# Optimization experiments

Measured on AMD Instinct MI355X. Metric: run time of the kernel, lower is better.

## Reference

```python
import jax, jax.numpy as jnp
import numpy as np

D = 1024
K = 256
B = 8192


def setup_inputs() -> dict:
    key = jax.random.key(0)
    kx, kw, kd, kp = jax.random.split(key, 4)
    x = jax.random.normal(kx, (B, D), dtype=jnp.float32)
    # scale weights ~1/sqrt(d) so the 11-matmul chain stays numerically sane
    Ws = jax.random.normal(kw, (10, D, D), dtype=jnp.float32) / jnp.sqrt(jnp.float32(D))
    W_dec = jax.random.normal(kd, (D, K), dtype=jnp.float32) / jnp.sqrt(jnp.float32(K))
    perm = jax.random.randint(kp, (K,), 0, D, dtype=jnp.int64)
    return {"x": x, "Ws": Ws, "W_dec": W_dec, "perm": perm}


def reference(x, Ws, W_dec, perm):
    # torch nn.Linear(d,d,bias=False): y = x @ W.T
    # source applies fc1..fc9, then fc9 AGAIN, then fc10 (11 matmuls, 10 weights)
    order = list(range(9)) + [8, 9]
    h = x
    for i in order:
        h = h @ Ws[i].T  # [B, D]
    y = h[:, perm]        # vectorized gather, replaces per-row python loop [B, K]
    out = y @ W_dec.T     # fc_decode: [B, D]
    return out
```

## Files before the change

kernel.cpp:

```cpp
#include <hip/hip_runtime.h>
#include <stdint.h>
#include <stddef.h>

typedef __bf16 bf16;
typedef __bf16 bf16x8 __attribute__((ext_vector_type(8)));
typedef float f32x4 __attribute__((ext_vector_type(4)));

__device__ __forceinline__ void global_to_lds16(const void* g, void* l) {
  const __attribute__((address_space(1))) unsigned* gp =
      reinterpret_cast<const __attribute__((address_space(1))) unsigned*>(
          reinterpret_cast<uintptr_t>(g));
  __attribute__((address_space(3))) unsigned* lp =
      reinterpret_cast<__attribute__((address_space(3))) unsigned*>(
          reinterpret_cast<uintptr_t>(l));
  __builtin_amdgcn_global_load_lds(gp, lp, 16, 0, 0);
}

struct PrepArgs {
  const float* cvt_src[5]; bf16* cvt_dst[5];
  const float* tr_src[6];  bf16* tr_dst[6];
  const float* x; bf16* xbf;
  const float* Wdec; const int* praw; bf16* Gbf;
};

__global__ __launch_bounds__(256) void prep_all(PrepArgs p) {
  __shared__ alignas(16) char smem[64 * 65 * 2];
  const int b = blockIdx.x;
  const int tid = threadIdx.x;

  if (b < 2560) {
    const int m = b >> 9, blk = b & 511;
    const float* __restrict__ src = p.cvt_src[m];
    bf16* __restrict__ dst = p.cvt_dst[m];
    const int i = (blk * 256 + tid) * 8;
    float4 a = *(const float4*)(src + i);
    float4 c = *(const float4*)(src + i + 4);
    bf16x8 o;
    o[0] = (bf16)a.x; o[1] = (bf16)a.y; o[2] = (bf16)a.z; o[3] = (bf16)a.w;
    o[4] = (bf16)c.x; o[5] = (bf16)c.y; o[6] = (bf16)c.z; o[7] = (bf16)c.w;
    *(bf16x8*)(dst + i) = o;
  } else if (b < 4096) {
    const int t = b - 2560;
    const int m = t >> 8, r = t & 255;
    const float* __restrict__ src = p.tr_src[m];
    bf16* __restrict__ dst = p.tr_dst[m];
    bf16(*tile)[65] = reinterpret_cast<bf16(*)[65]>(smem);
    const int bx = (r & 15) * 64;
    const int by = (r >> 4) * 64;
    const int tx = tid & 63;
    const int ty4 = tid >> 6;
#pragma unroll
    for (int rr = 0; rr < 16; rr++) {
      int row = ty4 * 16 + rr;
      tile[row][tx] = (bf16)src[(size_t)(by + row) * 1024 + bx + tx];
    }
    __syncthreads();
#pragma unroll
    for (int rr = 0; rr < 16; rr++) {
      int row = ty4 * 16 + rr;
      dst[(size_t)(bx + row) * 1024 + by + tx] = tile[tx][row];
    }
  } else if (b < 8192) {
    const int blk = b - 4096;
    const int i = (blk * 256 + tid) * 8;
    float4 a = *(const float4*)(p.x + i);
    float4 c = *(const float4*)(p.x + i + 4);
    bf16x8 o;
    o[0] = (bf16)a.x; o[1] = (bf16)a.y; o[2] = (bf16)a.z; o[3] = (bf16)a.w;
    o[4] = (bf16)c.x; o[5] = (bf16)c.y; o[6] = (bf16)c.z; o[7] = (bf16)c.w;
    *(bf16x8*)(p.xbf + i) = o;
  } else {
    const int j = b - 8192;
    float* row = (float*)smem;
    int* perm_l = (int*)(smem + 4096);
    int* nzp = (int*)(smem + 4096 + 1024);
#pragma unroll
    for (int c = 0; c < 4; c++) row[tid * 4 + c] = 0.f;
    if (tid == 0) *nzp = 0;
    __syncthreads();
    if (tid < 128 && p.praw[2 * tid + 1] != 0) atomicOr(nzp, 1);
    __syncthreads();
    const int is64 = (*nzp == 0);
    perm_l[tid] = is64 ? p.praw[2 * tid] : p.praw[tid];
    __syncthreads();
    atomicAdd(&row[perm_l[tid]], p.Wdec[(size_t)j * 256 + tid]);
    __syncthreads();
#pragma unroll
    for (int c = 0; c < 4; c++)
      p.Gbf[(size_t)j * 1024 + tid * 4 + c] = (bf16)row[tid * 4 + c];
  }
}

struct GemmBatch { const bf16* A[6]; const bf16* B[6]; bf16* C[6]; };

__global__ __launch_bounds__(256) void gemm64_nt(GemmBatch bt) {
  const bf16* __restrict__ A = bt.A[blockIdx.z];
  const bf16* __restrict__ B = bt.B[blockIdx.z];
  bf16* __restrict__ C = bt.C[blockIdx.z];

  __shared__ bf16 As[64 * 32];
  __shared__ bf16 Bs[64 * 32];

  const int tid = threadIdx.x;
  const int wave = tid >> 6, lane = tid & 63;
  const int quad = lane >> 4, l16 = lane & 15;
  const int rowBase = blockIdx.y * 64;
  const int colBase = blockIdx.x * 64;
  const int waveM = (wave >> 1) * 32, waveN = (wave & 1) * 32;

  const int e = tid * 8;
  const int sr = e >> 5, sc = e & 31;
  const bf16* Ag = A + (size_t)(rowBase + sr) * 1024 + sc;
  const bf16* Bg = B + (size_t)(colBase + sr) * 1024 + sc;
  char* AsB = (char*)As + wave * 1024;
  char* BsB = (char*)Bs + wave * 1024;

  f32x4 acc[2][2] = {};

  for (int k0 = 0; k0 < 1024; k0 += 32) {
    global_to_lds16(Ag + k0, AsB);
    global_to_lds16(Bg + k0, BsB);
    __syncthreads();
    bf16x8 af[2], bfr[2];
#pragma unroll
    for (int mi = 0; mi < 2; mi++)
      af[mi] = *(const bf16x8*)(As + (waveM + mi * 16 + l16) * 32 + quad * 8);
#pragma unroll
    for (int ni = 0; ni < 2; ni++)
      bfr[ni] = *(const bf16x8*)(Bs + (waveN + ni * 16 + l16) * 32 + quad * 8);
#pragma unroll
    for (int mi = 0; mi < 2; mi++)
#pragma unroll
      for (int ni = 0; ni < 2; ni++)
        acc[mi][ni] = __builtin_amdgcn_mfma_f32_16x16x32_bf16(af[mi], bfr[ni],
                                                              acc[mi][ni], 0, 0, 0);
    __syncthreads();
  }

  bf16* Cb = C + (size_t)(rowBase + waveM) * 1024 + colBase + waveN;
#pragma unroll
  for (int mi = 0; mi < 2; mi++)
#pragma unroll
    for (int ni = 0; ni < 2; ni++)
#pragma unroll
      for (int r = 0; r < 4; r++)
        Cb[(size_t)(mi * 16 + quad * 4 + r) * 1024 + ni * 16 + l16] =
            (bf16)acc[mi][ni][r];
}

__global__ __launch_bounds__(256) void gemm128_nt_f32(const bf16* __restrict__ A,
                                                      const bf16* __restrict__ B,
                                                      float* __restrict__ C) {
  __shared__ bf16 As[128 * 32];
  __shared__ bf16 Bs[128 * 32];

  const int tid = threadIdx.x;
  const int wave = tid >> 6, lane = tid & 63;
  const int quad = lane >> 4, l16 = lane & 15;
  const int rowBase = blockIdx.y * 128;
  const int colBase = blockIdx.x * 128;
  const int waveM = (wave >> 1) * 64, waveN = (wave & 1) * 64;

  const int e = tid * 8;
  const int sr = e >> 5, sc = e & 31;
  const bf16* Ag0 = A + (size_t)(rowBase + sr) * 1024 + sc;
  const bf16* Ag1 = Ag0 + (size_t)64 * 1024;
  const bf16* Bg0 = B + (size_t)(colBase + sr) * 1024 + sc;
  const bf16* Bg1 = Bg0 + (size_t)64 * 1024;
  char* AsB0 = (char*)As + wave * 1024;
  char* AsB1 = AsB0 + 4096;
  char* BsB0 = (char*)Bs + wave * 1024;
  char* BsB1 = BsB0 + 4096;

  f32x4 acc[4][4] = {};

  for (int k0 = 0; k0 < 1024; k0 += 32) {
    global_to_lds16(Ag0 + k0, AsB0);
    global_to_lds16(Ag1 + k0, AsB1);
    global_to_lds16(Bg0 + k0, BsB0);
    global_to_lds16(Bg1 + k0, BsB1);
    __syncthreads();
    bf16x8 af[4], bfr[4];
#pragma unroll
    for (int mi = 0; mi < 4; mi++)
      af[mi] = *(const bf16x8*)(As + (waveM + mi * 16 + l16) * 32 + quad * 8);
#pragma unroll
    for (int ni = 0; ni < 4; ni++)
      bfr[ni] = *(const bf16x8*)(Bs + (waveN + ni * 16 + l16) * 32 + quad * 8);
#pragma unroll
    for (int mi = 0; mi < 4; mi++)
#pragma unroll
      for (int ni = 0; ni < 4; ni++)
        acc[mi][ni] = __builtin_amdgcn_mfma_f32_16x16x32_bf16(af[mi], bfr[ni],
                                                              acc[mi][ni], 0, 0, 0);
    __syncthreads();
  }

  float* Cb = C + (size_t)(rowBase + waveM) * 1024 + colBase + waveN;
#pragma unroll
  for (int mi = 0; mi < 4; mi++)
#pragma unroll
    for (int ni = 0; ni < 4; ni++)
#pragma unroll
      for (int r = 0; r < 4; r++)
        Cb[(size_t)(mi * 16 + quad * 4 + r) * 1024 + ni * 16 + l16] =
            acc[mi][ni][r];
}

extern "C" void kernel_launch(void* const* d_in, const int* in_sizes, int n_in,
                              void* d_out, int out_size, void* d_ws, size_t ws_size,
                              hipStream_t stream) {
  const float* x    = (const float*)d_in[0];
  const float* Wsrc = (const float*)d_in[1];
  const float* Wdec = (const float*)d_in[2];
  const int*   praw = (const int*)d_in[3];
  float* out = (float*)d_out;

  constexpr size_t MAT  = 1024ull * 1024ull;
  constexpr size_t SLOT = 2ull * 1024 * 1024;

  char* ws = (char*)d_ws;
  bf16* Wrm[5];
  for (int i = 0; i < 5; i++) Wrm[i] = (bf16*)(ws + (size_t)i * SLOT);
  bf16* Wt[6];
  for (int i = 0; i < 6; i++) Wt[i] = (bf16*)(ws + (size_t)(5 + i) * SLOT);
  bf16* Gbf = (bf16*)(ws + 11 * SLOT);
  bf16* xbf = (bf16*)(ws + 12 * SLOT);
  bf16* P[6];
  for (int i = 0; i < 6; i++) P[i] = (bf16*)(ws + (size_t)(20 + i) * SLOT);
  bf16* Q[3];
  for (int i = 0; i < 3; i++) Q[i] = (bf16*)(ws + (size_t)(26 + i) * SLOT);
  bf16* Rb = (bf16*)(ws + 29 * SLOT);
  bf16* Fb = (bf16*)(ws + 30 * SLOT);

  PrepArgs pa;
  const int rmIdx[5] = {1, 3, 5, 7, 8};
  for (int i = 0; i < 5; i++) { pa.cvt_src[i] = Wsrc + (size_t)rmIdx[i] * MAT; pa.cvt_dst[i] = Wrm[i]; }
  const int trIdx[6] = {0, 2, 4, 6, 8, 9};
  for (int i = 0; i < 6; i++) { pa.tr_src[i] = Wsrc + (size_t)trIdx[i] * MAT; pa.tr_dst[i] = Wt[i]; }
  pa.x = x; pa.xbf = xbf; pa.Wdec = Wdec; pa.praw = praw; pa.Gbf = Gbf;
  prep_all<<<dim3(9216), 256, 0, stream>>>(pa);

  GemmBatch L1;
  const bf16* l1a[6] = {Gbf, Wt[4], Wrm[3], Wt[2], Wrm[1], Wt[0]};
  const bf16* l1b[6] = {Wt[5], Wrm[4], Wt[3], Wrm[2], Wt[1], Wrm[0]};
  for (int i = 0; i < 6; i++) { L1.A[i] = l1a[i]; L1.B[i] = l1b[i]; L1.C[i] = P[i]; }
  gemm64_nt<<<dim3(16, 16, 6), 256, 0, stream>>>(L1);

  GemmBatch L2;
  const bf16* l2a[3] = {P[0], P[3], P[5]};
  const bf16* l2b[3] = {P[1], P[2], P[4]};
  for (int i = 0; i < 3; i++) { L2.A[i] = l2a[i]; L2.B[i] = l2b[i]; L2.C[i] = Q[i]; }
  gemm64_nt<<<dim3(16, 16, 3), 256, 0, stream>>>(L2);

  GemmBatch L3{};
  L3.A[0] = Q[0]; L3.B[0] = Q[1]; L3.C[0] = Rb;
  gemm64_nt<<<dim3(16, 16, 1), 256, 0, stream>>>(L3);

  GemmBatch L4{};
  L4.A[0] = Rb; L4.B[0] = Q[2]; L4.C[0] = Fb;
  gemm64_nt<<<dim3(16, 16, 1), 256, 0, stream>>>(L4);

  gemm128_nt_f32<<<dim3(8, 64), 256, 0, stream>>>(xbf, Fb, out);

  (void)in_sizes; (void)n_in; (void)out_size; (void)ws_size;
}
```

Measured before the change: 222.5 us.

## Use 128x128 tiles for weight-chain GEMMs and fold x conversion into first GEMM launch

The weight-product tree GEMMs move from 64x64 tiles to the shared 128x128 MFMA body, which raises data reuse per block. The catch is far fewer blocks: 64 per 1024x1024 product, on a device with many CUs. The fp32-to-bf16 conversion of x is moved out of the prep kernel and into the first-level GEMM launch as trailing blocks. The aim is to overlap that memory-bound work with the compute-bound GEMM blocks. The risk is poor GPU occupancy in the serial L3/L4 stages, where only 64 blocks run.

```diff
diff --git a/kernel.cpp b/kernel.cpp
--- a/kernel.cpp
+++ b/kernel.cpp
@@ -16,10 +16,70 @@
   __builtin_amdgcn_global_load_lds(gp, lp, 16, 0, 0);
 }
 
+template <typename OutT>
+__device__ __forceinline__ void gemm128_body(const bf16* __restrict__ A,
+                                             const bf16* __restrict__ B,
+                                             OutT* __restrict__ C,
+                                             int bx, int by) {
+  __shared__ bf16 As[128 * 32];
+  __shared__ bf16 Bs[128 * 32];
+
+  const int tid = threadIdx.x;
+  const int wave = tid >> 6, lane = tid & 63;
+  const int quad = lane >> 4, l16 = lane & 15;
+  const int rowBase = by * 128;
+  const int colBase = bx * 128;
+  const int waveM = (wave >> 1) * 64, waveN = (wave & 1) * 64;
+
+  const int e = tid * 8;
+  const int sr = e >> 5, sc = e & 31;
+  const bf16* Ag0 = A + (size_t)(rowBase + sr) * 1024 + sc;
+  const bf16* Ag1 = Ag0 + (size_t)64 * 1024;
+  const bf16* Bg0 = B + (size_t)(colBase + sr) * 1024 + sc;
+  const bf16* Bg1 = Bg0 + (size_t)64 * 1024;
+  char* AsB0 = (char*)As + wave * 1024;
+  char* AsB1 = AsB0 + 4096;
+  char* BsB0 = (char*)Bs + wave * 1024;
+  char* BsB1 = BsB0 + 4096;
+
+  f32x4 acc[4][4] = {};
+
+  for (int k0 = 0; k0 < 1024; k0 += 32) {
+    global_to_lds16(Ag0 + k0, AsB0);
+    global_to_lds16(Ag1 + k0, AsB1);
+    global_to_lds16(Bg0 + k0, BsB0);
+    global_to_lds16(Bg1 + k0, BsB1);
+    __syncthreads();
+    bf16x8 af[4], bfr[4];
+#pragma unroll
+    for (int mi = 0; mi < 4; mi++)
+      af[mi] = *(const bf16x8*)(As + (waveM + mi * 16 + l16) * 32 + quad * 8);
+#pragma unroll
+    for (int ni = 0; ni < 4; ni++)
+      bfr[ni] = *(const bf16x8*)(Bs + (waveN + ni * 16 + l16) * 32 + quad * 8);
+#pragma unroll
+    for (int mi = 0; mi < 4; mi++)
+#pragma unroll
+      for (int ni = 0; ni < 4; ni++)
+        acc[mi][ni] = __builtin_amdgcn_mfma_f32_16x16x32_bf16(af[mi], bfr[ni],
+                                                              acc[mi][ni], 0, 0, 0);
+    __syncthreads();
+  }
+
+  OutT* Cb = C + (size_t)(rowBase + waveM) * 1024 + colBase + waveN;
+#pragma unroll
+  for (int mi = 0; mi < 4; mi++)
+#pragma unroll
+    for (int ni = 0; ni < 4; ni++)
+#pragma unroll
+      for (int r = 0; r < 4; r++)
+        Cb[(size_t)(mi * 16 + quad * 4 + r) * 1024 + ni * 16 + l16] =
+            (OutT)acc[mi][ni][r];
+}
+
 struct PrepArgs {
   const float* cvt_src[5]; bf16* cvt_dst[5];
   const float* tr_src[6];  bf16* tr_dst[6];
-  const float* x; bf16* xbf;
   const float* Wdec; const int* praw; bf16* Gbf;
 };
 
@@ -60,17 +120,8 @@
       int row = ty4 * 16 + rr;
       dst[(size_t)(bx + row) * 1024 + by + tx] = tile[tx][row];
     }
-  } else if (b < 8192) {
-    const int blk = b - 4096;
-    const int i = (blk * 256 + tid) * 8;
-    float4 a = *(const float4*)(p.x + i);
-    float4 c = *(const float4*)(p.x + i + 4);
-    bf16x8 o;
-    o[0] = (bf16)a.x; o[1] = (bf16)a.y; o[2] = (bf16)a.z; o[3] = (bf16)a.w;
-    o[4] = (bf16)c.x; o[5] = (bf16)c.y; o[6] = (bf16)c.z; o[7] = (bf16)c.w;
-    *(bf16x8*)(p.xbf + i) = o;
   } else {
-    const int j = b - 8192;
+    const int j = b - 4096;
     float* row = (float*)smem;
     int* perm_l = (int*)(smem + 4096);
     int* nzp = (int*)(smem + 4096 + 1024);
@@ -91,120 +142,39 @@
   }
 }
 
-struct GemmBatch { const bf16* A[6]; const bf16* B[6]; bf16* C[6]; };
-
-__global__ __launch_bounds__(256) void gemm64_nt(GemmBatch bt) {
-  const bf16* __restrict__ A = bt.A[blockIdx.z];
-  const bf16* __restrict__ B = bt.B[blockIdx.z];
-  bf16* __restrict__ C = bt.C[blockIdx.z];
-
-  __shared__ bf16 As[64 * 32];
-  __shared__ bf16 Bs[64 * 32];
-
-  const int tid = threadIdx.x;
-  const int wave = tid >> 6, lane = tid & 63;
-  const int quad = lane >> 4, l16 = lane & 15;
-  const int rowBase = blockIdx.y * 64;
-  const int colBase = blockIdx.x * 64;
-  const int waveM = (wave >> 1) * 32, waveN = (wave & 1) * 32;
-
-  const int e = tid * 8;
-  const int sr = e >> 5, sc = e & 31;
-  const bf16* Ag = A + (size_t)(rowBase + sr) * 1024 + sc;
-  const bf16* Bg = B + (size_t)(colBase + sr) * 1024 + sc;
-  char* AsB = (char*)As + wave * 1024;
-  char* BsB = (char*)Bs + wave * 1024;
-
-  f32x4 acc[2][2] = {};
-
-  for (int k0 = 0; k0 < 1024; k0 += 32) {
-    global_to_lds16(Ag + k0, AsB);
-    global_to_lds16(Bg + k0, BsB);
-    __syncthreads();
-    bf16x8 af[2], bfr[2];
-#pragma unroll
-    for (int mi = 0; mi < 2; mi++)
-      af[mi] = *(const bf16x8*)(As + (waveM + mi * 16 + l16) * 32 + quad * 8);
-#pragma unroll
-    for (int ni = 0; ni < 2; ni++)
-      bfr[ni] = *(const bf16x8*)(Bs + (waveN + ni * 16 + l16) * 32 + quad * 8);
-#pragma unroll
-    for (int mi = 0; mi < 2; mi++)
-#pragma unroll
-      for (int ni = 0; ni < 2; ni++)
-        acc[mi][ni] = __builtin_amdgcn_mfma_f32_16x16x32_bf16(af[mi], bfr[ni],
-                                                              acc[mi][ni], 0, 0, 0);
-    __syncthreads();
+struct L1Args {
+  const bf16* A[6]; const bf16* B[6]; bf16* C[6];
+  const float* x; bf16* xbf;
+};
+
+__global__ __launch_bounds__(256) void l1_gemm_xcvt(L1Args a) {
+  const int b = blockIdx.x;
+  if (b < 384) {
+    const int z = b >> 6, t = b & 63;
+    gemm128_body<bf16>(a.A[z], a.B[z], a.C[z], t & 7, t >> 3);
+  } else {
+    const int i = ((b - 384) * 256 + (int)threadIdx.x) * 8;
+    float4 v0 = *(const float4*)(a.x + i);
+    float4 v1 = *(const float4*)(a.x + i + 4);
+    bf16x8 o;
+    o[0] = (bf16)v0.x; o[1] = (bf16)v0.y; o[2] = (bf16)v0.z; o[3] = (bf16)v0.w;
+    o[4] = (bf16)v1.x; o[5] = (bf16)v1.y; o[6] = (bf16)v1.z; o[7] = (bf16)v1.w;
+    *(bf16x8*)(a.xbf + i) = o;
   }
-
-  bf16* Cb = C + (size_t)(rowBase + waveM) * 1024 + colBase + waveN;
-#pragma unroll
-  for (int mi = 0; mi < 2; mi++)
-#pragma unroll
-    for (int ni = 0; ni < 2; ni++)
-#pragma unroll
-      for (int r = 0; r < 4; r++)
-        Cb[(size_t)(mi * 16 + quad * 4 + r) * 1024 + ni * 16 + l16] =
-            (bf16)acc[mi][ni][r];
-}
-
-__global__ __launch_bounds__(256) void gemm128_nt_f32(const bf16* __restrict__ A,
-                                                      const bf16* __restrict__ B,
-                                                      float* __restrict__ C) {
-  __shared__ bf16 As[128 * 32];
-  __shared__ bf16 Bs[128 * 32];
-
-  const int tid = threadIdx.x;
-  const int wave = tid >> 6, lane = tid & 63;
-  const int quad = lane >> 4, l16 = lane & 15;
-  const int rowBase = blockIdx.y * 128;
-  const int colBase = blockIdx.x * 128;
-  const int waveM = (wave >> 1) * 64, waveN = (wave & 1) * 64;
-
-  const int e = tid * 8;
-  const int sr = e >> 5, sc = e & 31;
-  const bf16* Ag0 = A + (size_t)(rowBase + sr) * 1024 + sc;
-  const bf16* Ag1 = Ag0 + (size_t)64 * 1024;
-  const bf16* Bg0 = B + (size_t)(colBase + sr) * 1024 + sc;
-  const bf16* Bg1 = Bg0 + (size_t)64 * 1024;
-  char* AsB0 = (char*)As + wave * 1024;
-  char* AsB1 = AsB0 + 4096;
-  char* BsB0 = (char*)Bs + wave * 1024;
-  char* BsB1 = BsB0 + 4096;
-
-  f32x4 acc[4][4] = {};
-
-  for (int k0 = 0; k0 < 1024; k0 += 32) {
-    global_to_lds16(Ag0 + k0, AsB0);
-    global_to_lds16(Ag1 + k0, AsB1);
-    global_to_lds16(Bg0 + k0, BsB0);
-    global_to_lds16(Bg1 + k0, BsB1);
-    __syncthreads();
-    bf16x8 af[4], bfr[4];
-#pragma unroll
-    for (int mi = 0; mi < 4; mi++)
-      af[mi] = *(const bf16x8*)(As + (waveM + mi * 16 + l16) * 32 + quad * 8);
-#pragma unroll
-    for (int ni = 0; ni < 4; ni++)
-      bfr[ni] = *(const bf16x8*)(Bs + (waveN + ni * 16 + l16) * 32 + quad * 8);
-#pragma unroll
-    for (int mi = 0; mi < 4; mi++)
-#pragma unroll
-      for (int ni = 0; ni < 4; ni++)
-        acc[mi][ni] = __builtin_amdgcn_mfma_f32_16x16x32_bf16(af[mi], bfr[ni],
-                                                              acc[mi][ni], 0, 0, 0);
-    __syncthreads();
-  }
-
-  float* Cb = C + (size_t)(rowBase + waveM) * 1024 + colBase + waveN;
-#pragma unroll
-  for (int mi = 0; mi < 4; mi++)
-#pragma unroll
-    for (int ni = 0; ni < 4; ni++)
-#pragma unroll
-      for (int r = 0; r < 4; r++)
-        Cb[(size_t)(mi * 16 + quad * 4 + r) * 1024 + ni * 16 + l16] =
-            acc[mi][ni][r];
+}
+
+struct GemmBatch { const bf16* A[3]; const bf16* B[3]; bf16* C[3]; };
+
+__global__ __launch_bounds__(256) void tree_gemm(GemmBatch bt) {
+  const int b = blockIdx.x;
+  const int z = b >> 6, t = b & 63;
+  gemm128_body<bf16>(bt.A[z], bt.B[z], bt.C[z], t & 7, t >> 3);
+}
+
+__global__ __launch_bounds__(256) void final_gemm(const bf16* __restrict__ A,
+                                                  const bf16* __restrict__ B,
+                                                  float* __restrict__ C) {
+  gemm128_body<float>(A, B, C, blockIdx.x, blockIdx.y);
 }
 
 extern "C" void kernel_launch(void* const* d_in, const int* in_sizes, int n_in,
@@ -238,30 +208,31 @@
   for (int i = 0; i < 5; i++) { pa.cvt_src[i] = Wsrc + (size_t)rmIdx[i] * MAT; pa.cvt_dst[i] = Wrm[i]; }
   const int trIdx[6] = {0, 2, 4, 6, 8, 9};
   for (int i = 0; i < 6; i++) { pa.tr_src[i] = Wsrc + (size_t)trIdx[i] * MAT; pa.tr_dst[i] = Wt[i]; }
-  pa.x = x; pa.xbf = xbf; pa.Wdec = Wdec; pa.praw = praw; pa.Gbf = Gbf;
-  prep_all<<<dim3(9216), 256, 0, stream>>>(pa);
-
-  GemmBatch L1;
+  pa.Wdec = Wdec; pa.praw = praw; pa.Gbf = Gbf;
+  prep_all<<<dim3(5120), 256, 0, stream>>>(pa);
+
+  L1Args l1;
   const bf16* l1a[6] = {Gbf, Wt[4], Wrm[3], Wt[2], Wrm[1], Wt[0]};
   const bf16* l1b[6] = {Wt[5], Wrm[4], Wt[3], Wrm[2], Wt[1], Wrm[0]};
-  for (int i = 0; i < 6; i++) { L1.A[i] = l1a[i]; L1.B[i] = l1b[i]; L1.C[i] = P[i]; }
-  gemm64_nt<<<dim3(16, 16, 6), 256, 0, stream>>>(L1);
+  for (int i = 0; i < 6; i++) { l1.A[i] = l1a[i]; l1.B[i] = l1b[i]; l1.C[i] = P[i]; }
+  l1.x = x; l1.xbf = xbf;
+  l1_gemm_xcvt<<<dim3(4480), 256, 0, stream>>>(l1);
 
   GemmBatch L2;
   const bf16* l2a[3] = {P[0], P[3], P[5]};
   const bf16* l2b[3] = {P[1], P[2], P[4]};
   for (int i = 0; i < 3; i++) { L2.A[i] = l2a[i]; L2.B[i] = l2b[i]; L2.C[i] = Q[i]; }
-  gemm64_nt<<<dim3(16, 16, 3), 256, 0, stream>>>(L2);
+  tree_gemm<<<dim3(192), 256, 0, stream>>>(L2);
 
   GemmBatch L3{};
   L3.A[0] = Q[0]; L3.B[0] = Q[1]; L3.C[0] = Rb;
-  gemm64_nt<<<dim3(16, 16, 1), 256, 0, stream>>>(L3);
+  tree_gemm<<<dim3(64), 256, 0, stream>>>(L3);
 
   GemmBatch L4{};
   L4.A[0] = Rb; L4.B[0] = Q[2]; L4.C[0] = Fb;
-  gemm64_nt<<<dim3(16, 16, 1), 256, 0, stream>>>(L4);
-
-  gemm128_nt_f32<<<dim3(8, 64), 256, 0, stream>>>(xbf, Fb, out);
+  tree_gemm<<<dim3(64), 256, 0, stream>>>(L4);
+
+  final_gemm<<<dim3(8, 64), 256, 0, stream>>>(xbf, Fb, out);
 
   (void)in_sizes; (void)n_in; (void)out_size; (void)ws_size;
 }
```

Result: slower. 231.7 us (+4.2%).
